# Kernel optimization log

Measured on AMD Instinct MI355X. Metric: run time of the kernel, lower is better.

The kernel has to match this reference:

```python
import jax, jax.numpy as jnp
import numpy as np

B, N, NR, D = 1024, 100000, 500, 200
OC, FW = 32, 9          # out_channels, filt_w (filt_h is always 1)
L = D - FW + 1          # 192, conv output width
EPS = 1e-5


def setup_inputs() -> dict:
    key = jax.random.key(0)
    ks = jax.random.split(key, 22)
    inp = {
        "e1_idx": jax.random.randint(ks[0], (B,), 0, N),
        "r_idx": jax.random.randint(ks[1], (B,), 0, NR),
        "E": jax.random.normal(ks[2], (N, D), jnp.float32) * 0.1,
        "R": jax.random.normal(ks[3], (NR, D), jnp.float32) * 0.1,
        "W_fc": jax.random.normal(ks[4], (OC * L, D), jnp.float32) * 0.02,
        "b_fc": jnp.zeros((D,), jnp.float32),
        "W_fc1": jax.random.normal(ks[5], (D, OC * FW), jnp.float32) * 0.05,
        "b_fc1": jnp.zeros((OC * FW,), jnp.float32),
        "bn0_g": jax.random.uniform(ks[6], (1,), jnp.float32, 0.5, 1.5),
        "bn0_b": jax.random.normal(ks[7], (1,), jnp.float32) * 0.1,
        "bn0_m": jax.random.normal(ks[8], (1,), jnp.float32) * 0.1,
        "bn0_v": jax.random.uniform(ks[9], (1,), jnp.float32, 0.5, 1.5),
        "bn1_g": jax.random.uniform(ks[10], (OC,), jnp.float32, 0.5, 1.5),
        "bn1_b": jax.random.normal(ks[11], (OC,), jnp.float32) * 0.1,
        "bn1_m": jax.random.normal(ks[12], (OC,), jnp.float32) * 0.1,
        "bn1_v": jax.random.uniform(ks[13], (OC,), jnp.float32, 0.5, 1.5),
        "bn2_g": jax.random.uniform(ks[14], (D,), jnp.float32, 0.5, 1.5),
        "bn2_b": jax.random.normal(ks[15], (D,), jnp.float32) * 0.1,
        "bn2_m": jax.random.normal(ks[16], (D,), jnp.float32) * 0.1,
        "bn2_v": jax.random.uniform(ks[17], (D,), jnp.float32, 0.5, 1.5),
        "b": jnp.zeros((N,), jnp.float32),
    }
    return inp


def reference(e1_idx, r_idx, E, R, W_fc, b_fc, W_fc1, b_fc1,
              bn0_g, bn0_b, bn0_m, bn0_v,
              bn1_g, bn1_b, bn1_m, bn1_v,
              bn2_g, bn2_b, bn2_m, bn2_v, b):
    # embeddings
    e1 = E[e1_idx]                       # [B, D]  (the [B,1,1,D] image)
    r = R[r_idx]                         # [B, D]
    # bn0 over the single input channel (eval mode, running stats)
    x = (e1 - bn0_m) * (bn0_g / jnp.sqrt(bn0_v + EPS)) + bn0_b   # [B, D]
    # hypernetwork: per-sample filters
    k = (r @ W_fc1 + b_fc1).reshape(B, OC, FW)                    # [B, OC, FW]
    # per-sample grouped conv == sliding-window batched small matmul
    idx = jnp.arange(L)[:, None] + jnp.arange(FW)[None, :]        # [L, FW]
    win = x[:, idx]                                               # [B, L, FW]
    y = jnp.einsum('blw,bow->bol', win, k)                        # [B, OC, L]
    # bn1 over OC channels (eval)
    y = (y - bn1_m[:, None]) * (bn1_g / jnp.sqrt(bn1_v + EPS))[:, None] + bn1_b[:, None]
    # fc (torch Linear: x @ W.T + b, W_fc is [fc_len, D])
    h = y.reshape(B, OC * L) @ W_fc + b_fc                        # [B, D]
    # bn2 over D features (eval) + relu
    h = (h - bn2_m) * (bn2_g / jnp.sqrt(bn2_v + EPS)) + bn2_b
    h = jax.nn.relu(h)
    # score against all entities
    logits = h @ E.T + b                                          # [B, N]
    return jax.nn.sigmoid(logits)
```

## Files before the change

kernel.cpp:

```cpp
#include <hip/hip_runtime.h>

#define B_    1024
#define N_    100000
#define NP_   100096
#define NR_   500
#define D_    200
#define KP_   224
#define OC_   32
#define FW_   9
#define L_    192
#define OCL_  6144
#define KS_   16
#define KCH_  384
#define NT_   1564
#define EPS_  1e-5f

typedef __attribute__((ext_vector_type(8))) short  bf16x8;
typedef __attribute__((ext_vector_type(4))) float  f32x4;

static __device__ __forceinline__ unsigned short f2bf(float x) {
    unsigned int u = __float_as_uint(x);
    unsigned int r = (u + 0x7FFFu + ((u >> 16) & 1u)) >> 16;
    return (unsigned short)r;
}

__global__ __launch_bounds__(256) void k1(
    const int* __restrict__ e1_idx, const int* __restrict__ r_idx,
    const float* __restrict__ E, const float* __restrict__ R,
    const float* __restrict__ W_fc1, const float* __restrict__ b_fc1,
    const float* __restrict__ W_fc,
    const float* __restrict__ bn0_g, const float* __restrict__ bn0_b,
    const float* __restrict__ bn0_m, const float* __restrict__ bn0_v,
    const float* __restrict__ bn1_g, const float* __restrict__ bn1_b,
    const float* __restrict__ bn1_m, const float* __restrict__ bn1_v,
    unsigned short* __restrict__ y_bf, unsigned short* __restrict__ Wt_bf)
{
    const int tid = threadIdx.x;
    const int bid = blockIdx.x;

    if (bid < B_) {
        __shared__ float x_lds[D_];
        __shared__ float r_lds[D_];
        __shared__ float k_lds[OC_ * FW_];
        __shared__ float s1_lds[OC_], t1_lds[OC_];

        const int b = bid;
        const float s0 = bn0_g[0] / sqrtf(bn0_v[0] + EPS_);
        const float c0 = bn0_b[0] - bn0_m[0] * s0;

        if (tid < D_) {
            x_lds[tid] = E[(long)e1_idx[b] * D_ + tid] * s0 + c0;
            r_lds[tid] = R[(long)r_idx[b] * D_ + tid];
        } else if (tid >= 224) {
            int o = tid - 224;
            float s1 = bn1_g[o] / sqrtf(bn1_v[o] + EPS_);
            s1_lds[o] = s1;
            t1_lds[o] = bn1_b[o] - bn1_m[o] * s1;
        }
        __syncthreads();

        for (int j = tid; j < OC_ * FW_; j += 256) {
            float acc = b_fc1[j];
            #pragma unroll 4
            for (int d = 0; d < D_; ++d)
                acc += r_lds[d] * W_fc1[d * (OC_ * FW_) + j];
            k_lds[j] = acc * s1_lds[j / FW_];
        }
        __syncthreads();

        unsigned short* yrow = y_bf + (long)b * OCL_;
        for (int idx = tid; idx < OCL_; idx += 256) {
            int o = idx / L_;
            int l = idx - o * L_;
            const float* kp = &k_lds[o * FW_];
            float acc = t1_lds[o];
            #pragma unroll
            for (int w = 0; w < FW_; ++w)
                acc += x_lds[l + w] * kp[w];
            yrow[idx] = f2bf(acc);
        }
    } else {
        __shared__ float t_lds[64][65];
        const int wb = bid - B_;
        const int k0 = (wb % 96) * 64;
        const int d0 = (wb / 96) * 64;
        const int c  = tid & 63;
        const int r4 = tid >> 6;
        #pragma unroll
        for (int i = 0; i < 16; ++i) {
            int row = i * 4 + r4;
            t_lds[row][c] = (d0 + c < D_) ? W_fc[(long)(k0 + row) * D_ + d0 + c] : 0.f;
        }
        __syncthreads();
        #pragma unroll
        for (int i = 0; i < 16; ++i) {
            int drow = i * 4 + r4;
            Wt_bf[(long)(d0 + drow) * OCL_ + k0 + c] = f2bf(t_lds[c][drow]);
        }
    }
}

__global__ __launch_bounds__(256) void kB(
    const unsigned short* __restrict__ y_bf, const unsigned short* __restrict__ Wt_bf,
    float* __restrict__ pre)
{
    const int wave = threadIdx.x >> 6;
    const int lane = threadIdx.x & 63;
    const int quad = lane >> 4;
    const int lc   = lane & 15;

    const int m0 = blockIdx.x * 128 + wave * 32;
    const int n0 = blockIdx.y * 64;
    const int kb = blockIdx.z * KCH_;

    f32x4 acc[2][4] = {};

    const short* a0p = (const short*)y_bf + (long)(m0 + lc) * OCL_ + kb + quad * 8;
    const short* a1p = a0p + 16 * OCL_;

    #pragma unroll
    for (int k0 = 0; k0 < KCH_; k0 += 32) {
        bf16x8 a0 = *(const bf16x8*)(a0p + k0);
        bf16x8 a1 = *(const bf16x8*)(a1p + k0);
        #pragma unroll
        for (int t = 0; t < 4; ++t) {
            bf16x8 bv = *(const bf16x8*)((const short*)Wt_bf
                         + (long)(n0 + t * 16 + lc) * OCL_ + kb + k0 + quad * 8);
            acc[0][t] = __builtin_amdgcn_mfma_f32_16x16x32_bf16(a0, bv, acc[0][t], 0, 0, 0);
            acc[1][t] = __builtin_amdgcn_mfma_f32_16x16x32_bf16(a1, bv, acc[1][t], 0, 0, 0);
        }
    }

    #pragma unroll
    for (int t = 0; t < 4; ++t) {
        int d = n0 + t * 16 + lc;
        if (d < KP_) {
            #pragma unroll
            for (int mi = 0; mi < 2; ++mi)
                #pragma unroll
                for (int r = 0; r < 4; ++r) {
                    int m = m0 + mi * 16 + quad * 4 + r;
                    pre[((long)blockIdx.z * B_ + m) * KP_ + d] = acc[mi][t][r];
                }
        }
    }
}

__global__ __launch_bounds__(256) void kB2(
    const float* __restrict__ pre, const float* __restrict__ b_fc,
    const float* __restrict__ bn2_g, const float* __restrict__ bn2_b,
    const float* __restrict__ bn2_m, const float* __restrict__ bn2_v,
    unsigned short* __restrict__ h_bf)
{
    int id = blockIdx.x * 256 + threadIdx.x;
    if (id >= B_ * KP_) return;
    int b = id / KP_;
    int d = id - b * KP_;
    float h = 0.f;
    if (d < D_) {
        float s = 0.f;
        #pragma unroll
        for (int sp = 0; sp < KS_; ++sp)
            s += pre[(long)sp * B_ * KP_ + id];
        float s2 = bn2_g[d] / sqrtf(bn2_v[d] + EPS_);
        h = (s + b_fc[d] - bn2_m[d]) * s2 + bn2_b[d];
        h = fmaxf(h, 0.f);
    }
    h_bf[id] = f2bf(h);
}

__global__ __launch_bounds__(256) void kC(
    const unsigned short* __restrict__ h_bf, const float* __restrict__ E,
    const float* __restrict__ bias, float* __restrict__ out)
{
    __shared__ short smem[64 * 256];

    const int tid  = threadIdx.x;
    const int wave = tid >> 6;
    const int lane = tid & 63;
    const int quad = lane >> 4;
    const int lc   = lane & 15;

    const int bid = blockIdx.x;
    const int g   = (bid & 7) * NT_ + (bid >> 3);
    const int m0  = (g & 7) * 128 + wave * 32;
    const int n0  = (g >> 3) * 64;

    {
        #pragma unroll
        for (int i = 0; i < 14; ++i) {
            int u   = tid + i * 256;
            int row = u / 56;
            int s8  = u - row * 56;
            int n   = n0 + row;
            ushort4 o = {0, 0, 0, 0};
            if (n < N_ && s8 < 50) {
                float4 v = *(const float4*)&E[(long)n * D_ + s8 * 4];
                o.x = f2bf(v.x); o.y = f2bf(v.y); o.z = f2bf(v.z); o.w = f2bf(v.w);
            }
            int c16 = s8 >> 1, half = s8 & 1;
            *(ushort4*)&smem[row * 256 + ((c16 ^ (row & 7)) << 3) + half * 4] = o;
        }
    }
    __syncthreads();

    f32x4 acc[2][4] = {};

    const short* hbase0 = (const short*)h_bf + (long)(m0 + lc) * KP_ + quad * 8;
    const short* hbase1 = hbase0 + 16 * KP_;

    #pragma unroll
    for (int k0 = 0; k0 < KP_; k0 += 32) {
        bf16x8 a0 = *(const bf16x8*)(hbase0 + k0);
        bf16x8 a1 = *(const bf16x8*)(hbase1 + k0);
        const int cbase = (k0 >> 3) + quad;
        #pragma unroll
        for (int t = 0; t < 4; ++t) {
            int row = t * 16 + lc;
            int c   = cbase ^ (row & 7);
            bf16x8 bv = *(const bf16x8*)&smem[row * 256 + c * 8];
            acc[0][t] = __builtin_amdgcn_mfma_f32_16x16x32_bf16(a0, bv, acc[0][t], 0, 0, 0);
            acc[1][t] = __builtin_amdgcn_mfma_f32_16x16x32_bf16(a1, bv, acc[1][t], 0, 0, 0);
        }
    }

    __syncthreads();
    float* fw = (float*)smem + wave * 2048;

    #pragma unroll
    for (int t = 0; t < 4; ++t) {
        int n = n0 + t * 16 + lc;
        float bv = (n < N_) ? bias[n] : 0.f;
        #pragma unroll
        for (int mi = 0; mi < 2; ++mi)
            #pragma unroll
            for (int r = 0; r < 4; ++r) {
                int rl = mi * 16 + quad * 4 + r;
                fw[rl * 64 + t * 16 + lc] = acc[mi][t][r] + bv;
            }
    }

    #pragma unroll
    for (int j = 0; j < 8; ++j) {
        int u  = lane + j * 64;
        int rl = u >> 4;
        int c4 = u & 15;
        int n  = n0 + c4 * 4;
        if (n < N_) {
            float4 v = *(const float4*)&fw[rl * 64 + c4 * 4];
            float4 o;
            o.x = 1.f / (1.f + __expf(-v.x));
            o.y = 1.f / (1.f + __expf(-v.y));
            o.z = 1.f / (1.f + __expf(-v.z));
            o.w = 1.f / (1.f + __expf(-v.w));
            *(float4*)&out[(long)(m0 + rl) * N_ + n] = o;
        }
    }
}

extern "C" void kernel_launch(void* const* d_in, const int* in_sizes, int n_in,
                              void* d_out, int out_size, void* d_ws, size_t ws_size,
                              hipStream_t stream) {
    const int*   e1_idx = (const int*)d_in[0];
    const int*   r_idx  = (const int*)d_in[1];
    const float* E      = (const float*)d_in[2];
    const float* R      = (const float*)d_in[3];
    const float* W_fc   = (const float*)d_in[4];
    const float* b_fc   = (const float*)d_in[5];
    const float* W_fc1  = (const float*)d_in[6];
    const float* b_fc1  = (const float*)d_in[7];
    const float* bn0_g  = (const float*)d_in[8];
    const float* bn0_b  = (const float*)d_in[9];
    const float* bn0_m  = (const float*)d_in[10];
    const float* bn0_v  = (const float*)d_in[11];
    const float* bn1_g  = (const float*)d_in[12];
    const float* bn1_b  = (const float*)d_in[13];
    const float* bn1_m  = (const float*)d_in[14];
    const float* bn1_v  = (const float*)d_in[15];
    const float* bn2_g  = (const float*)d_in[16];
    const float* bn2_b  = (const float*)d_in[17];
    const float* bn2_m  = (const float*)d_in[18];
    const float* bn2_v  = (const float*)d_in[19];
    const float* bias   = (const float*)d_in[20];
    float* out = (float*)d_out;

    char* base = (char*)d_ws;
    unsigned short* y_bf  = (unsigned short*)(base);
    float*          pre   = (float*)(base + 12582912L);
    unsigned short* Wt_bf = (unsigned short*)(base + 27262976L);
    unsigned short* h_bf  = (unsigned short*)(base + 44843008L);

    k1<<<B_ + 384, 256, 0, stream>>>(e1_idx, r_idx, E, R, W_fc1, b_fc1, W_fc,
                                     bn0_g, bn0_b, bn0_m, bn0_v,
                                     bn1_g, bn1_b, bn1_m, bn1_v,
                                     y_bf, Wt_bf);
    kB<<<dim3(8, 4, KS_), 256, 0, stream>>>(y_bf, Wt_bf, pre);
    kB2<<<(B_ * KP_ + 255) / 256, 256, 0, stream>>>(pre, b_fc, bn2_g, bn2_b, bn2_m, bn2_v, h_bf);
    kC<<<8 * NT_, 256, 0, stream>>>(h_bf, E, bias, out);
}
```

Measured before the change: 733.3 us.

## Reuse converted entity tile across all batch tiles in scoring kernel

The scoring kernel now assigns one 64-entity slice per block and loops over all eight 128-row batch tiles, so the E tile is loaded and converted to bf16 in LDS only once instead of eight times. The grid shrinks by a factor of eight, and the epilogue uses a separate, padded per-wave LDS staging buffer to avoid bank conflicts. The trade-offs are fewer blocks in flight, higher LDS usage per block and less latency hiding within the serial loop.

```diff
diff --git a/kernel.cpp b/kernel.cpp
--- a/kernel.cpp
+++ b/kernel.cpp
@@ -2,7 +2,6 @@
 
 #define B_    1024
 #define N_    100000
-#define NP_   100096
 #define NR_   500
 #define D_    200
 #define KP_   224
@@ -12,7 +11,7 @@
 #define OCL_  6144
 #define KS_   16
 #define KCH_  384
-#define NT_   1564
+#define NT_   1563
 #define EPS_  1e-5f
 
 typedef __attribute__((ext_vector_type(8))) short  bf16x8;
@@ -173,87 +172,91 @@
     const unsigned short* __restrict__ h_bf, const float* __restrict__ E,
     const float* __restrict__ bias, float* __restrict__ out)
 {
-    __shared__ short smem[64 * 256];
+    __shared__ short smemB[64 * 256];
+    __shared__ float smemE[4][32 * 68];
 
     const int tid  = threadIdx.x;
     const int wave = tid >> 6;
     const int lane = tid & 63;
     const int quad = lane >> 4;
     const int lc   = lane & 15;
-
-    const int bid = blockIdx.x;
-    const int g   = (bid & 7) * NT_ + (bid >> 3);
-    const int m0  = (g & 7) * 128 + wave * 32;
-    const int n0  = (g >> 3) * 64;
-
-    {
-        #pragma unroll
-        for (int i = 0; i < 14; ++i) {
-            int u   = tid + i * 256;
-            int row = u / 56;
-            int s8  = u - row * 56;
-            int n   = n0 + row;
-            ushort4 o = {0, 0, 0, 0};
-            if (n < N_ && s8 < 50) {
-                float4 v = *(const float4*)&E[(long)n * D_ + s8 * 4];
-                o.x = f2bf(v.x); o.y = f2bf(v.y); o.z = f2bf(v.z); o.w = f2bf(v.w);
-            }
-            int c16 = s8 >> 1, half = s8 & 1;
-            *(ushort4*)&smem[row * 256 + ((c16 ^ (row & 7)) << 3) + half * 4] = o;
-        }
+    const int n0   = blockIdx.x * 64;
+
+    #pragma unroll
+    for (int i = 0; i < 14; ++i) {
+        int u   = tid + i * 256;
+        int row = u / 56;
+        int s8  = u - row * 56;
+        int n   = n0 + row;
+        ushort4 o = {0, 0, 0, 0};
+        if (n < N_ && s8 < 50) {
+            float4 v = *(const float4*)&E[(long)n * D_ + s8 * 4];
+            o.x = f2bf(v.x); o.y = f2bf(v.y); o.z = f2bf(v.z); o.w = f2bf(v.w);
+        }
+        int c16 = s8 >> 1, half = s8 & 1;
+        *(ushort4*)&smemB[row * 256 + ((c16 ^ (row & 7)) << 3) + half * 4] = o;
     }
     __syncthreads();
 
-    f32x4 acc[2][4] = {};
-
-    const short* hbase0 = (const short*)h_bf + (long)(m0 + lc) * KP_ + quad * 8;
-    const short* hbase1 = hbase0 + 16 * KP_;
-
-    #pragma unroll
-    for (int k0 = 0; k0 < KP_; k0 += 32) {
-        bf16x8 a0 = *(const bf16x8*)(hbase0 + k0);
-        bf16x8 a1 = *(const bf16x8*)(hbase1 + k0);
-        const int cbase = (k0 >> 3) + quad;
-        #pragma unroll
-        for (int t = 0; t < 4; ++t) {
-            int row = t * 16 + lc;
-            int c   = cbase ^ (row & 7);
-            bf16x8 bv = *(const bf16x8*)&smem[row * 256 + c * 8];
-            acc[0][t] = __builtin_amdgcn_mfma_f32_16x16x32_bf16(a0, bv, acc[0][t], 0, 0, 0);
-            acc[1][t] = __builtin_amdgcn_mfma_f32_16x16x32_bf16(a1, bv, acc[1][t], 0, 0, 0);
-        }
-    }
-
-    __syncthreads();
-    float* fw = (float*)smem + wave * 2048;
-
+    float bv[4];
     #pragma unroll
     for (int t = 0; t < 4; ++t) {
         int n = n0 + t * 16 + lc;
-        float bv = (n < N_) ? bias[n] : 0.f;
-        #pragma unroll
-        for (int mi = 0; mi < 2; ++mi)
+        bv[t] = (n < N_) ? bias[n] : 0.f;
+    }
+
+    float* fw = smemE[wave];
+
+    for (int mi = 0; mi < 8; ++mi) {
+        const int m0 = mi * 128 + wave * 32;
+
+        const short* hb = (const short*)h_bf + (long)(m0 + lc) * KP_ + quad * 8;
+        bf16x8 a0v[7], a1v[7];
+        #pragma unroll
+        for (int kk = 0; kk < 7; ++kk) {
+            a0v[kk] = *(const bf16x8*)(hb + kk * 32);
+            a1v[kk] = *(const bf16x8*)(hb + 16 * KP_ + kk * 32);
+        }
+
+        f32x4 acc[2][4] = {};
+        #pragma unroll
+        for (int kk = 0; kk < 7; ++kk) {
+            const int cbase = kk * 4 + quad;
             #pragma unroll
-            for (int r = 0; r < 4; ++r) {
-                int rl = mi * 16 + quad * 4 + r;
-                fw[rl * 64 + t * 16 + lc] = acc[mi][t][r] + bv;
+            for (int t = 0; t < 4; ++t) {
+                int row = t * 16 + lc;
+                int c   = cbase ^ (row & 7);
+                bf16x8 bvv = *(const bf16x8*)&smemB[row * 256 + c * 8];
+                acc[0][t] = __builtin_amdgcn_mfma_f32_16x16x32_bf16(a0v[kk], bvv, acc[0][t], 0, 0, 0);
+                acc[1][t] = __builtin_amdgcn_mfma_f32_16x16x32_bf16(a1v[kk], bvv, acc[1][t], 0, 0, 0);
             }
-    }
-
-    #pragma unroll
-    for (int j = 0; j < 8; ++j) {
-        int u  = lane + j * 64;
-        int rl = u >> 4;
-        int c4 = u & 15;
-        int n  = n0 + c4 * 4;
-        if (n < N_) {
-            float4 v = *(const float4*)&fw[rl * 64 + c4 * 4];
-            float4 o;
-            o.x = 1.f / (1.f + __expf(-v.x));
-            o.y = 1.f / (1.f + __expf(-v.y));
-            o.z = 1.f / (1.f + __expf(-v.z));
-            o.w = 1.f / (1.f + __expf(-v.w));
-            *(float4*)&out[(long)(m0 + rl) * N_ + n] = o;
+        }
+
+        #pragma unroll
+        for (int t = 0; t < 4; ++t)
+            #pragma unroll
+            for (int mii = 0; mii < 2; ++mii)
+                #pragma unroll
+                for (int r = 0; r < 4; ++r) {
+                    int rl = mii * 16 + quad * 4 + r;
+                    fw[rl * 68 + t * 16 + lc] = acc[mii][t][r] + bv[t];
+                }
+
+        #pragma unroll
+        for (int j = 0; j < 8; ++j) {
+            int u  = lane + j * 64;
+            int rl = u >> 4;
+            int c4 = u & 15;
+            int n  = n0 + c4 * 4;
+            if (n < N_) {
+                float4 v = *(const float4*)&fw[rl * 68 + c4 * 4];
+                float4 o;
+                o.x = 1.f / (1.f + __expf(-v.x));
+                o.y = 1.f / (1.f + __expf(-v.y));
+                o.z = 1.f / (1.f + __expf(-v.z));
+                o.w = 1.f / (1.f + __expf(-v.w));
+                *(float4*)&out[(long)(m0 + rl) * N_ + n] = o;
+            }
         }
     }
 }
@@ -296,5 +299,5 @@
                                      y_bf, Wt_bf);
     kB<<<dim3(8, 4, KS_), 256, 0, stream>>>(y_bf, Wt_bf, pre);
     kB2<<<(B_ * KP_ + 255) / 256, 256, 0, stream>>>(pre, b_fc, bn2_g, bn2_b, bn2_m, bn2_v, h_bf);
-    kC<<<8 * NT_, 256, 0, stream>>>(h_bf, E, bias, out);
-}
+    kC<<<NT_, 256, 0, stream>>>(h_bf, E, bias, out);
+}
```

Measured after the change: 640.6 us. -12.6%, faster.
